# Kernel optimization log

Hardware: AMD Instinct MI355X
Metric: run time of the kernel (lower is better)

The kernel has to match this reference:

```python
import jax, jax.numpy as jnp
import numpy as np

N, E, C, RB, H = 10000, 160000, 64, 8, 64
AVG_NEIGH = 16.0


def _sph(v):
    # component-normalized real spherical harmonics l=1,2,3 of unit vectors v [E,3]
    x, y, z = v[..., 0], v[..., 1], v[..., 2]
    s3, s5, s15 = 3.0 ** 0.5, 5.0 ** 0.5, 15.0 ** 0.5
    y1 = s3 * jnp.stack([x, y, z], -1)  # [E,3]
    y2 = jnp.stack([
        s15 * x * y,
        s15 * y * z,
        0.5 * s5 * (3.0 * z * z - 1.0),
        s15 * x * z,
        0.5 * s15 * (x * x - y * y),
    ], -1)  # [E,5]
    c1 = (35.0 / 8.0) ** 0.5
    c2 = 105.0 ** 0.5
    c3 = (21.0 / 8.0) ** 0.5
    c4 = (7.0 ** 0.5) / 2.0
    y3 = jnp.stack([
        c1 * y * (3.0 * x * x - y * y),
        c2 * x * y * z,
        c3 * y * (5.0 * z * z - 1.0),
        c4 * z * (5.0 * z * z - 3.0),
        c3 * x * (5.0 * z * z - 1.0),
        0.5 * c2 * z * (x * x - y * y),
        c1 * x * (x * x - y * y),
    ], -1)  # [E,7]
    return y1, y2, y3


def setup_inputs() -> dict:
    key = jax.random.key(0)
    ks = jax.random.split(key, 12)
    inp = {
        'vectors': jax.random.normal(ks[0], (E, 3), jnp.float32),
        'node_feats': jax.random.normal(ks[1], (N, C), jnp.float32),
        'radial_embedding': jax.random.normal(ks[2], (E, RB), jnp.float32),
        'W_up': jax.random.normal(ks[3], (C, C), jnp.float32) / np.sqrt(C),
        'mlp_w1': jax.random.normal(ks[4], (RB, H), jnp.float32) / np.sqrt(RB),
        'mlp_w2': jax.random.normal(ks[5], (H, H), jnp.float32) / np.sqrt(H),
        'mlp_w3': jax.random.normal(ks[6], (H, H), jnp.float32) / np.sqrt(H),
        'mlp_w4': jax.random.normal(ks[7], (H, 4 * C), jnp.float32) / np.sqrt(H),
        'W_down': jax.random.normal(ks[8], (4, C, C), jnp.float32) / np.sqrt(C),
        'senders': jax.random.randint(ks[9], (E,), 0, N, jnp.int32),
        'receivers': jax.random.randint(ks[10], (E,), 0, N, jnp.int32),
    }
    return inp


def reference(vectors, node_feats, radial_embedding, W_up, mlp_w1, mlp_w2, mlp_w3, mlp_w4, W_down, senders, receivers):
    n = node_feats.shape[0]
    # linear_up (scalars: plain channel mixing)
    x = node_feats @ W_up                                   # [N,C]
    sf = x[senders]                                         # [E,C] gather
    u = vectors / (jnp.linalg.norm(vectors, axis=-1, keepdims=True) + 1e-12)
    y1, y2, y3 = _sph(u)
    # radial MLP -> per-irrep mixing weights [E, 4C]
    h = jax.nn.silu(radial_embedding @ mlp_w1)
    h = jax.nn.silu(h @ mlp_w2)
    h = jax.nn.silu(h @ mlp_w3)
    mix = h @ mlp_w4
    m0, m1, m2, m3 = jnp.split(mix, 4, axis=-1)             # each [E,C]
    # tensor product of Cx0e with Y_l -> Cx(l), scaled by radial mix
    msg0 = sf * m0                                          # [E,C]
    msg1 = (sf * m1)[:, :, None] * y1[:, None, :]           # [E,C,3]
    msg2 = (sf * m2)[:, :, None] * y2[:, None, :]           # [E,C,5]
    msg3 = (sf * m3)[:, :, None] * y3[:, None, :]           # [E,C,7]
    inv = 1.0 / jnp.sqrt(jnp.asarray(AVG_NEIGH, msg0.dtype))
    seg = lambda m: jax.ops.segment_sum(m, receivers, num_segments=n) * inv
    o0, o1, o2, o3 = seg(msg0), seg(msg1), seg(msg2), seg(msg3)
    # linear_down: per-l channel mixing
    o0 = o0 @ W_down[0]
    o1 = jnp.einsum('ncm,cd->ndm', o1, W_down[1])
    o2 = jnp.einsum('ncm,cd->ndm', o2, W_down[2])
    o3 = jnp.einsum('ncm,cd->ndm', o3, W_down[3])
    return jnp.concatenate([o0, o1.reshape(n, -1), o2.reshape(n, -1), o3.reshape(n, -1)], axis=-1)  # [N, 16C]
```

## Files before the change

### kernel.cpp

```cpp
#include <hip/hip_runtime.h>
#include <math.h>

#define CC 64
typedef _Float16 f16;
typedef _Float16 half8_t __attribute__((ext_vector_type(8)));
typedef float f32x4 __attribute__((ext_vector_type(4)));

__device__ __forceinline__ float silu_f(float v) {
    return v * __builtin_amdgcn_rcpf(1.0f + __expf(-v));
}

__global__ __launch_bounds__(256) void k_pre(
        const float* __restrict__ nf, const float* __restrict__ Wup,
        float* __restrict__ x, int N,
        const float* __restrict__ w1, const float* __restrict__ w2,
        const float* __restrict__ w3, const float* __restrict__ w4,
        const float* __restrict__ Wd,
        f16* __restrict__ wT1, f16* __restrict__ wT2,
        f16* __restrict__ wT3, f16* __restrict__ wT4,
        float* __restrict__ wpack,
        const int* __restrict__ rcv, int* __restrict__ cnt, int E) {
    int nb_up = (N * CC + 255) >> 8;
    int b = blockIdx.x;
    if (b < nb_up) {
        int tid = b * 256 + threadIdx.x;
        if (tid >= N * CC) return;
        int n = tid >> 6;
        int j = tid & 63;
        const float* nfr = nf + (size_t)n * CC;
        float acc = 0.f;
#pragma unroll
        for (int k = 0; k < CC; ++k) acc += nfr[k] * Wup[k * CC + j];
        x[tid] = acc;
    } else if (b < nb_up + 168) {
        int i = (b - nb_up) * 256 + threadIdx.x;
        if (i < 2048) {
            int n = i >> 5, k = i & 31;
            wT1[i] = (k < 8) ? (f16)w1[k * 64 + n] : (f16)0.f;
        } else if (i < 6144) {
            int j = i - 2048; int n = j >> 6, k = j & 63;
            wT2[j] = (f16)w2[k * 64 + n];
        } else if (i < 10240) {
            int j = i - 6144; int n = j >> 6, k = j & 63;
            wT3[j] = (f16)w3[k * 64 + n];
        } else if (i < 26624) {
            int j = i - 10240; int l = j >> 12; int r = j & 4095;
            int n = r >> 6, k = r & 63;
            wT4[j] = (f16)w4[k * 256 + l * 64 + n];
        } else if (i < 43008) {
            int j = i - 26624;
            int pos = j >> 2;
            int comp = j & 3;
            wpack[j] = 0.25f * Wd[comp * 4096 + pos];
        }
    } else {
        int e = (b - nb_up - 168) * 256 + threadIdx.x;
        if (e < E) atomicAdd(&cnt[rcv[e]], 1);
    }
}

__global__ __launch_bounds__(1024) void k_scan(const int* __restrict__ cnt,
        int* __restrict__ off, int* __restrict__ cur, int N) {
    __shared__ int wsum[16];
    int t = threadIdx.x;
    int wave = t >> 6, lane = t & 63;
    int per = (N + 1023) >> 10;
    int i0 = t * per;
    int s = 0;
    for (int j = 0; j < per; ++j) {
        int i = i0 + j;
        if (i < N) s += cnt[i];
    }
    int sc = s;
#pragma unroll
    for (int d = 1; d < 64; d <<= 1) {
        int u = __shfl_up(sc, d, 64);
        if (lane >= d) sc += u;
    }
    if (lane == 63) wsum[wave] = sc;
    __syncthreads();
    if (wave == 0) {
        int v = (lane < 16) ? wsum[lane] : 0;
        int s2 = v;
#pragma unroll
        for (int d = 1; d < 16; d <<= 1) {
            int u = __shfl_up(s2, d, 64);
            if (lane >= d) s2 += u;
        }
        if (lane < 16) wsum[lane] = s2;
    }
    __syncthreads();
    int base = ((wave > 0) ? wsum[wave - 1] : 0) + (sc - s);
    int run = base;
    for (int j = 0; j < per; ++j) {
        int i = i0 + j;
        if (i < N) { off[i] = run; cur[i] = run; run += cnt[i]; }
    }
    if (t == 1023) off[N] = run;
}

__global__ void k_fill(const int* __restrict__ rcv, const int* __restrict__ snd,
                       const float* __restrict__ vec, int* __restrict__ cur,
                       int* __restrict__ eid, int* __restrict__ sndp,
                       float* __restrict__ yb, int E) {
    int e = blockIdx.x * blockDim.x + threadIdx.x;
    if (e >= E) return;
    int p = atomicAdd(&cur[rcv[e]], 1);
    eid[p] = e;
    sndp[p] = snd[e];

    float vx = vec[(size_t)e * 3 + 0];
    float vy = vec[(size_t)e * 3 + 1];
    float vz = vec[(size_t)e * 3 + 2];
    float nrm = sqrtf(vx * vx + vy * vy + vz * vz) + 1e-12f;
    float rinv = 1.0f / nrm;
    float ux = vx * rinv, uy = vy * rinv, uz = vz * rinv;

    const float s3 = 1.7320508075688772f;
    const float s5 = 2.2360679774997896f;
    const float s15 = 3.8729833462074170f;
    const float c1 = 2.0916500663351889f;
    const float c2 = 10.246950765959598f;
    const float c3 = 1.6201851746019651f;
    const float c4 = 1.3228756555322954f;

    float zz = uz * uz, xx = ux * ux, yy = uy * uy;
    float4 r0 = {1.0f, s3 * ux, s3 * uy, s3 * uz};
    float4 r1 = {s15 * ux * uy, s15 * uy * uz, 0.5f * s5 * (3.f * zz - 1.f),
                 s15 * ux * uz};
    float4 r2 = {0.5f * s15 * (xx - yy), c1 * uy * (3.f * xx - yy),
                 c2 * ux * uy * uz, c3 * uy * (5.f * zz - 1.f)};
    float4 r3 = {c4 * uz * (5.f * zz - 3.f), c3 * ux * (5.f * zz - 1.f),
                 0.5f * c2 * uz * (xx - yy), c1 * ux * (xx - yy)};
    float* yr = yb + (size_t)p * 16;
    *(float4*)(yr + 0)  = r0;
    *(float4*)(yr + 4)  = r1;
    *(float4*)(yr + 8)  = r2;
    *(float4*)(yr + 12) = r3;
}

__global__ __launch_bounds__(128) void k_mlp(const float* __restrict__ rad,
        const f16* __restrict__ wT1, const f16* __restrict__ wT2,
        const f16* __restrict__ wT3, const f16* __restrict__ wT4,
        const int* __restrict__ eid, const int* __restrict__ sndp,
        const float* __restrict__ x, f16* __restrict__ mixp, int E) {
    __shared__ f16 act[64][72];

    int t = threadIdx.x;
    int e0 = blockIdx.x * 64;
    int lane = t & 63;
    int wid = t >> 6;
    int m0 = wid * 32;
    int fm = lane & 15;
    int q  = lane >> 4;

    const half8_t hz = {0, 0, 0, 0, 0, 0, 0, 0};

    float4 sfa[4], sfb[4];
#pragma unroll
    for (int it = 0; it < 4; ++it) {
        int row = (lane >> 3) + it * 8;
        int ci = e0 + m0 + row;
        int s = (ci < E) ? sndp[ci] : 0;
        const float* xr = x + (size_t)s * 64 + (lane & 7) * 8;
        sfa[it] = *(const float4*)xr;
        sfb[it] = *(const float4*)(xr + 4);
    }

    half8_t a0 = hz, a1 = hz;
    if (q == 0) {
        int ci0 = e0 + m0 + fm;
        if (ci0 < E) {
            int e = eid[ci0];
            float4 p0 = *(const float4*)(rad + (size_t)e * 8);
            float4 p1 = *(const float4*)(rad + (size_t)e * 8 + 4);
            a0 = (half8_t){(f16)p0.x, (f16)p0.y, (f16)p0.z, (f16)p0.w,
                           (f16)p1.x, (f16)p1.y, (f16)p1.z, (f16)p1.w};
        }
        int ci1 = e0 + m0 + 16 + fm;
        if (ci1 < E) {
            int e = eid[ci1];
            float4 p0 = *(const float4*)(rad + (size_t)e * 8);
            float4 p1 = *(const float4*)(rad + (size_t)e * 8 + 4);
            a1 = (half8_t){(f16)p0.x, (f16)p0.y, (f16)p0.z, (f16)p0.w,
                           (f16)p1.x, (f16)p1.y, (f16)p1.z, (f16)p1.w};
        }
    }
#pragma unroll
    for (int nt = 0; nt < 4; ++nt) {
        half8_t b = *(const half8_t*)(wT1 + ((nt * 16 + fm) << 5) + q * 8);
        f32x4 c0 = {0.f, 0.f, 0.f, 0.f};
        c0 = __builtin_amdgcn_mfma_f32_16x16x32_f16(a0, b, c0, 0, 0, 0);
        f32x4 c1 = {0.f, 0.f, 0.f, 0.f};
        c1 = __builtin_amdgcn_mfma_f32_16x16x32_f16(a1, b, c1, 0, 0, 0);
#pragma unroll
        for (int r = 0; r < 4; ++r) {
            act[m0 + q * 4 + r][nt * 16 + fm]      = (f16)silu_f(c0[r]);
            act[m0 + 16 + q * 4 + r][nt * 16 + fm] = (f16)silu_f(c1[r]);
        }
    }

    auto loadA = [&](int mbase, int kc) -> half8_t {
        return *(const half8_t*)&act[mbase + fm][kc + q * 8];
    };

    const f16* wts[2] = {wT2, wT3};
#pragma unroll
    for (int L = 0; L < 2; ++L) {
        const f16* wT = wts[L];
        half8_t a00 = loadA(m0, 0),      a01 = loadA(m0, 32);
        half8_t a10 = loadA(m0 + 16, 0), a11 = loadA(m0 + 16, 32);
#pragma unroll
        for (int nt = 0; nt < 4; ++nt) {
            const f16* wr = wT + ((nt * 16 + fm) << 6);
            half8_t b0 = *(const half8_t*)(wr + q * 8);
            half8_t b1 = *(const half8_t*)(wr + 32 + q * 8);
            f32x4 c0 = {0.f, 0.f, 0.f, 0.f};
            c0 = __builtin_amdgcn_mfma_f32_16x16x32_f16(a00, b0, c0, 0, 0, 0);
            c0 = __builtin_amdgcn_mfma_f32_16x16x32_f16(a01, b1, c0, 0, 0, 0);
            f32x4 c1 = {0.f, 0.f, 0.f, 0.f};
            c1 = __builtin_amdgcn_mfma_f32_16x16x32_f16(a10, b0, c1, 0, 0, 0);
            c1 = __builtin_amdgcn_mfma_f32_16x16x32_f16(a11, b1, c1, 0, 0, 0);
#pragma unroll
            for (int r = 0; r < 4; ++r) {
                act[m0 + q * 4 + r][nt * 16 + fm]      = (f16)silu_f(c0[r]);
                act[m0 + 16 + q * 4 + r][nt * 16 + fm] = (f16)silu_f(c1[r]);
            }
        }
    }

    half8_t sfh[4];
#pragma unroll
    for (int it = 0; it < 4; ++it) {
        sfh[it] = (half8_t){(f16)sfa[it].x, (f16)sfa[it].y,
                            (f16)sfa[it].z, (f16)sfa[it].w,
                            (f16)sfb[it].x, (f16)sfb[it].y,
                            (f16)sfb[it].z, (f16)sfb[it].w};
    }

    half8_t A00 = loadA(m0, 0),      A01 = loadA(m0, 32);
    half8_t A10 = loadA(m0 + 16, 0), A11 = loadA(m0 + 16, 32);

#pragma unroll
    for (int l = 0; l < 4; ++l) {
        const f16* wT = wT4 + (l << 12);
#pragma unroll
        for (int nt = 0; nt < 4; ++nt) {
            const f16* wr = wT + ((nt * 16 + fm) << 6);
            half8_t b0 = *(const half8_t*)(wr + q * 8);
            half8_t b1 = *(const half8_t*)(wr + 32 + q * 8);
            f32x4 c0 = {0.f, 0.f, 0.f, 0.f};
            c0 = __builtin_amdgcn_mfma_f32_16x16x32_f16(A00, b0, c0, 0, 0, 0);
            c0 = __builtin_amdgcn_mfma_f32_16x16x32_f16(A01, b1, c0, 0, 0, 0);
            f32x4 c1 = {0.f, 0.f, 0.f, 0.f};
            c1 = __builtin_amdgcn_mfma_f32_16x16x32_f16(A10, b0, c1, 0, 0, 0);
            c1 = __builtin_amdgcn_mfma_f32_16x16x32_f16(A11, b1, c1, 0, 0, 0);
#pragma unroll
            for (int r = 0; r < 4; ++r) {
                act[m0 + q * 4 + r][nt * 16 + fm]      = (f16)c0[r];
                act[m0 + 16 + q * 4 + r][nt * 16 + fm] = (f16)c1[r];
            }
        }
#pragma unroll
        for (int it = 0; it < 4; ++it) {
            int row = (lane >> 3) + it * 8;
            int ci = e0 + m0 + row;
            if (ci < E) {
                half8_t v = *(const half8_t*)&act[m0 + row][(lane & 7) * 8];
                half8_t w = v * sfh[it];
                *(half8_t*)&mixp[(size_t)ci * 256 + l * 64 + (lane & 7) * 8] = w;
            }
        }
    }
}

__global__ __launch_bounds__(256) void k_gather(
        const f16* __restrict__ mixp, const float* __restrict__ yb,
        const int* __restrict__ off, const f32x4* __restrict__ wpack,
        float* __restrict__ out, int N) {
    __shared__ float sbuf[4][64 * 20];
    __shared__ float ybs[4][16][16];
    int wv = threadIdx.x >> 6;
    int lane = threadIdx.x & 63;
    int n = blockIdx.x * 4 + wv;
    if (n >= N) return;

    float o[16];
#pragma unroll
    for (int i = 0; i < 16; ++i) o[i] = 0.f;

    auto process = [&](int i, int j) {
        const float* yr = &ybs[wv][j][0];
        f32x4 A  = *(const f32x4*)(yr + 0);
        f32x4 B  = *(const f32x4*)(yr + 4);
        f32x4 Cv = *(const f32x4*)(yr + 8);
        f32x4 D  = *(const f32x4*)(yr + 12);
        const f16* mr = mixp + (size_t)i * 256;
        float t0 = (float)mr[lane];
        float t1 = (float)mr[64 + lane];
        float t2 = (float)mr[128 + lane];
        float t3 = (float)mr[192 + lane];
        o[0]  += t0;
        o[1]  += t1 * A.y;
        o[2]  += t1 * A.z;
        o[3]  += t1 * A.w;
        o[4]  += t2 * B.x;
        o[5]  += t2 * B.y;
        o[6]  += t2 * B.z;
        o[7]  += t2 * B.w;
        o[8]  += t2 * Cv.x;
        o[9]  += t3 * Cv.y;
        o[10] += t3 * Cv.z;
        o[11] += t3 * Cv.w;
        o[12] += t3 * D.x;
        o[13] += t3 * D.y;
        o[14] += t3 * D.z;
        o[15] += t3 * D.w;
    };

    int beg = off[n], end = off[n + 1];
    for (int cb = beg; cb < end; cb += 16) {
        int m = end - cb; if (m > 16) m = 16;
        if (lane < m * 4) {
            f32x4 v = *(const f32x4*)(yb + (size_t)cb * 16 + lane * 4);
            *(f32x4*)&ybs[wv][lane >> 2][(lane & 3) * 4] = v;
        }
        int j = 0;
        for (; j + 1 < m; j += 2) { process(cb + j, j); process(cb + j + 1, j + 1); }
        if (j < m) process(cb + j, j);
    }

    float* sw = sbuf[wv];
#pragma unroll
    for (int a = 0; a < 4; ++a) {
        f32x4 vq = {o[4 * a + 0], o[4 * a + 1], o[4 * a + 2], o[4 * a + 3]};
        *(f32x4*)&sw[lane * 20 + 4 * a] = vq;
    }

    f32x4 dA = {0.f, 0.f, 0.f, 0.f}, dB = dA, dC = dA, dD = dA;
#pragma unroll 2
    for (int c = 0; c < 64; ++c) {
        f32x4 q0 = *(const f32x4*)&sw[c * 20 + 0];
        f32x4 q1 = *(const f32x4*)&sw[c * 20 + 4];
        f32x4 q2 = *(const f32x4*)&sw[c * 20 + 8];
        f32x4 q3 = *(const f32x4*)&sw[c * 20 + 12];
        f32x4 wp = wpack[c * 64 + lane];
        f32x4 wA = {wp.x, wp.y, wp.y, wp.y};
        f32x4 wC4 = {wp.z, wp.w, wp.w, wp.w};
        dA += q0 * wA;
        dB += q1 * wp.z;
        dC += q2 * wC4;
        dD += q3 * wp.w;
    }

    float* outr = out + (size_t)n * 1024;
    outr[lane] = dA[0];
#pragma unroll
    for (int m = 0; m < 3; ++m) outr[64 + lane * 3 + m] = dA[1 + m];
    outr[256 + lane * 5 + 0] = dB[0];
    outr[256 + lane * 5 + 1] = dB[1];
    outr[256 + lane * 5 + 2] = dB[2];
    outr[256 + lane * 5 + 3] = dB[3];
    outr[256 + lane * 5 + 4] = dC[0];
    outr[576 + lane * 7 + 0] = dC[1];
    outr[576 + lane * 7 + 1] = dC[2];
    outr[576 + lane * 7 + 2] = dC[3];
    outr[576 + lane * 7 + 3] = dD[0];
    outr[576 + lane * 7 + 4] = dD[1];
    outr[576 + lane * 7 + 5] = dD[2];
    outr[576 + lane * 7 + 6] = dD[3];
}

extern "C" void kernel_launch(void* const* d_in, const int* in_sizes, int n_in,
                              void* d_out, int out_size, void* d_ws, size_t ws_size,
                              hipStream_t stream) {
    const float* vectors    = (const float*)d_in[0];
    const float* node_feats = (const float*)d_in[1];
    const float* radial     = (const float*)d_in[2];
    const float* W_up       = (const float*)d_in[3];
    const float* w1         = (const float*)d_in[4];
    const float* w2         = (const float*)d_in[5];
    const float* w3         = (const float*)d_in[6];
    const float* w4         = (const float*)d_in[7];
    const float* Wd         = (const float*)d_in[8];
    const int*   snd        = (const int*)d_in[9];
    const int*   rcv        = (const int*)d_in[10];
    float* out = (float*)d_out;

    int E = in_sizes[9];
    int N = in_sizes[1] / CC;

    f16*   wT1   = (f16*)d_ws;
    f16*   wT2   = wT1 + 2048;
    f16*   wT3   = wT2 + 4096;
    f16*   wT4   = wT3 + 4096;
    float* wpack = (float*)(wT4 + 16384);
    float* x     = wpack + 16384;
    float* yb    = x + (size_t)N * 64;
    f16*   mixp  = (f16*)(yb + (size_t)E * 16);
    int*   cnt   = (int*)(mixp + (size_t)E * 256);
    int*   off   = cnt + N;
    int*   cur   = off + (N + 1);
    int*   eid   = cur + N;
    int*   sndp  = eid + E;

    hipMemsetAsync(cnt, 0, (size_t)N * sizeof(int), stream);

    int nb_up = (N * CC + 255) / 256;
    int nb_hist = (E + 255) / 256;
    k_pre<<<nb_up + 168 + nb_hist, 256, 0, stream>>>(
        node_feats, W_up, x, N, w1, w2, w3, w4, Wd,
        wT1, wT2, wT3, wT4, wpack, rcv, cnt, E);
    k_scan<<<1, 1024, 0, stream>>>(cnt, off, cur, N);
    k_fill<<<(E + 255) / 256, 256, 0, stream>>>(rcv, snd, vectors, cur, eid, sndp, yb, E);
    k_mlp<<<(E + 63) / 64, 128, 0, stream>>>(radial, wT1, wT2, wT3, wT4,
                                             eid, sndp, x, mixp, E);
    k_gather<<<(N + 3) / 4, 256, 0, stream>>>(mixp, yb, off,
                                              (const f32x4*)wpack, out, N);
}
```

Baseline: 217.1 us.

## Interleave per-edge mix buffer channel-major so gather loads one half4 per lane

Reorders the per-edge fp16 mix buffer from [l][channel] to [channel][l], so each lane in the gather kernel fetches all four irrep weights with a single 8-byte load instead of four scattered 2-byte loads. The MLP kernel now writes its final-layer outputs into a new shared staging tile in the interleaved order, split over two channel halves, and reloads the sender features in a matching lane mapping. This adds about 17 KB of shared memory per block and a more complex store path in the MLP kernel, which may lower occupancy there.

New measurement: 228.0 us. +5.0%, slower.

```diff
diff --git a/kernel.cpp b/kernel.cpp
--- a/kernel.cpp
+++ b/kernel.cpp
@@ -4,6 +4,7 @@
 #define CC 64
 typedef _Float16 f16;
 typedef _Float16 half8_t __attribute__((ext_vector_type(8)));
+typedef _Float16 half4_t __attribute__((ext_vector_type(4)));
 typedef float f32x4 __attribute__((ext_vector_type(4)));
 
 __device__ __forceinline__ float silu_f(float v) {
@@ -145,6 +146,7 @@
         const int* __restrict__ eid, const int* __restrict__ sndp,
         const float* __restrict__ x, f16* __restrict__ mixp, int E) {
     __shared__ f16 act[64][72];
+    __shared__ f16 zs[64][132];
 
     int t = threadIdx.x;
     int e0 = blockIdx.x * 64;
@@ -156,15 +158,16 @@
 
     const half8_t hz = {0, 0, 0, 0, 0, 0, 0, 0};
 
-    float4 sfa[4], sfb[4];
-#pragma unroll
-    for (int it = 0; it < 4; ++it) {
-        int row = (lane >> 3) + it * 8;
-        int ci = e0 + m0 + row;
+    float4 sf[2][4];
+#pragma unroll
+    for (int it = 0; it < 2; ++it) {
+        int ci = e0 + m0 + it * 16 + (lane >> 2);
         int s = (ci < E) ? sndp[ci] : 0;
-        const float* xr = x + (size_t)s * 64 + (lane & 7) * 8;
-        sfa[it] = *(const float4*)xr;
-        sfb[it] = *(const float4*)(xr + 4);
+        const float* xr = x + (size_t)s * 64 + (lane & 3) * 8;
+        sf[it][0] = *(const float4*)xr;
+        sf[it][1] = *(const float4*)(xr + 4);
+        sf[it][2] = *(const float4*)(xr + 32);
+        sf[it][3] = *(const float4*)(xr + 36);
     }
 
     half8_t a0 = hz, a1 = hz;
@@ -229,46 +232,49 @@
         }
     }
 
-    half8_t sfh[4];
-#pragma unroll
-    for (int it = 0; it < 4; ++it) {
-        sfh[it] = (half8_t){(f16)sfa[it].x, (f16)sfa[it].y,
-                            (f16)sfa[it].z, (f16)sfa[it].w,
-                            (f16)sfb[it].x, (f16)sfb[it].y,
-                            (f16)sfb[it].z, (f16)sfb[it].w};
-    }
-
     half8_t A00 = loadA(m0, 0),      A01 = loadA(m0, 32);
     half8_t A10 = loadA(m0 + 16, 0), A11 = loadA(m0 + 16, 32);
 
 #pragma unroll
-    for (int l = 0; l < 4; ++l) {
-        const f16* wT = wT4 + (l << 12);
-#pragma unroll
-        for (int nt = 0; nt < 4; ++nt) {
-            const f16* wr = wT + ((nt * 16 + fm) << 6);
-            half8_t b0 = *(const half8_t*)(wr + q * 8);
-            half8_t b1 = *(const half8_t*)(wr + 32 + q * 8);
-            f32x4 c0 = {0.f, 0.f, 0.f, 0.f};
-            c0 = __builtin_amdgcn_mfma_f32_16x16x32_f16(A00, b0, c0, 0, 0, 0);
-            c0 = __builtin_amdgcn_mfma_f32_16x16x32_f16(A01, b1, c0, 0, 0, 0);
-            f32x4 c1 = {0.f, 0.f, 0.f, 0.f};
-            c1 = __builtin_amdgcn_mfma_f32_16x16x32_f16(A10, b0, c1, 0, 0, 0);
-            c1 = __builtin_amdgcn_mfma_f32_16x16x32_f16(A11, b1, c1, 0, 0, 0);
-#pragma unroll
-            for (int r = 0; r < 4; ++r) {
-                act[m0 + q * 4 + r][nt * 16 + fm]      = (f16)c0[r];
-                act[m0 + 16 + q * 4 + r][nt * 16 + fm] = (f16)c1[r];
+    for (int h = 0; h < 2; ++h) {
+#pragma unroll
+        for (int l = 0; l < 4; ++l) {
+            const f16* wT = wT4 + (l << 12);
+#pragma unroll
+            for (int ntl = 0; ntl < 2; ++ntl) {
+                int nt = h * 2 + ntl;
+                const f16* wr = wT + ((nt * 16 + fm) << 6);
+                half8_t b0 = *(const half8_t*)(wr + q * 8);
+                half8_t b1 = *(const half8_t*)(wr + 32 + q * 8);
+                f32x4 c0 = {0.f, 0.f, 0.f, 0.f};
+                c0 = __builtin_amdgcn_mfma_f32_16x16x32_f16(A00, b0, c0, 0, 0, 0);
+                c0 = __builtin_amdgcn_mfma_f32_16x16x32_f16(A01, b1, c0, 0, 0, 0);
+                f32x4 c1 = {0.f, 0.f, 0.f, 0.f};
+                c1 = __builtin_amdgcn_mfma_f32_16x16x32_f16(A10, b0, c1, 0, 0, 0);
+                c1 = __builtin_amdgcn_mfma_f32_16x16x32_f16(A11, b1, c1, 0, 0, 0);
+#pragma unroll
+                for (int r = 0; r < 4; ++r) {
+                    zs[m0 + q * 4 + r][((ntl * 16 + fm) << 2) + l]      = (f16)c0[r];
+                    zs[m0 + 16 + q * 4 + r][((ntl * 16 + fm) << 2) + l] = (f16)c1[r];
+                }
             }
         }
 #pragma unroll
-        for (int it = 0; it < 4; ++it) {
-            int row = (lane >> 3) + it * 8;
-            int ci = e0 + m0 + row;
+        for (int it = 0; it < 2; ++it) {
+            int ci = e0 + m0 + it * 16 + (lane >> 2);
             if (ci < E) {
-                half8_t v = *(const half8_t*)&act[m0 + row][(lane & 7) * 8];
-                half8_t w = v * sfh[it];
-                *(half8_t*)&mixp[(size_t)ci * 256 + l * 64 + (lane & 7) * 8] = w;
+                const f16* zr = &zs[m0 + it * 16 + (lane >> 2)][(lane & 3) * 32];
+                f16* mp = mixp + (size_t)ci * 256 + (h * 32 + (lane & 3) * 8) * 4;
+#pragma unroll
+                for (int j = 0; j < 4; ++j) {
+                    half8_t v = *(const half8_t*)(zr + j * 8);
+                    float4 s4 = sf[it][h * 2 + (j >> 1)];
+                    float fa = (j & 1) ? s4.z : s4.x;
+                    float fb = (j & 1) ? s4.w : s4.y;
+                    f16 ha = (f16)fa, hb = (f16)fb;
+                    half8_t sm = {ha, ha, ha, ha, hb, hb, hb, hb};
+                    *(half8_t*)(mp + j * 8) = v * sm;
+                }
             }
         }
     }
@@ -295,11 +301,11 @@
         f32x4 B  = *(const f32x4*)(yr + 4);
         f32x4 Cv = *(const f32x4*)(yr + 8);
         f32x4 D  = *(const f32x4*)(yr + 12);
-        const f16* mr = mixp + (size_t)i * 256;
-        float t0 = (float)mr[lane];
-        float t1 = (float)mr[64 + lane];
-        float t2 = (float)mr[128 + lane];
-        float t3 = (float)mr[192 + lane];
+        half4_t mv = *(const half4_t*)(mixp + (size_t)i * 256 + lane * 4);
+        float t0 = (float)mv[0];
+        float t1 = (float)mv[1];
+        float t2 = (float)mv[2];
+        float t3 = (float)mv[3];
         o[0]  += t0;
         o[1]  += t1 * A.y;
         o[2]  += t1 * A.z;
```
